# Kernel optimization log

Measured on AMD Instinct MI355X. Metric: run time of the kernel, lower is better.

## Reference

```python
import jax, jax.numpy as jnp
import numpy as np

WS = 7        # window_size
HEADS = 4     # dim_in // dim_head = 256 // 64
DH = 64       # dim_head (for q/k)
SCALE = DH ** -0.5


def setup_inputs() -> dict:
    key = jax.random.key(0)
    k1, k2, k3 = jax.random.split(key, 3)
    x = jax.random.normal(k1, (32, 256, 56, 56), dtype=jnp.float32)
    qk_w = jax.random.normal(k2, (512, 256), dtype=jnp.float32) * 0.02  # 1x1 conv: (out_c, in_c)
    v_w = jax.random.normal(k3, (256, 256), dtype=jnp.float32) * 0.02
    return {"x": x, "qk_w": qk_w, "v_w": v_w}


def _forward(x, qk_w, v_w):
    B, C, H, W = x.shape
    pad_b = (WS - H % WS) % WS
    pad_r = (WS - W % WS) % WS
    x = jnp.pad(x, ((0, 0), (0, 0), (0, pad_b), (0, pad_r)))
    Hp, Wp = H + pad_b, W + pad_r
    n1, n2 = Hp // WS, Wp // WS

    # 1x1 convs (no bias): qk -> 2*C channels, v -> dim_mid channels with ReLU
    qk = jnp.einsum('bchw,oc->bohw', x, qk_w)
    v = jax.nn.relu(jnp.einsum('bchw,oc->bohw', x, v_w))

    # remote (dilated grid) partition: 'b c (h1 n1) (w1 n2) -> (b n1 n2) c h1 w1'
    def part_r(t):
        b, c = t.shape[:2]
        return t.reshape(b, c, WS, n1, WS, n2).transpose(0, 3, 5, 1, 2, 4).reshape(b * n1 * n2, c, WS, WS)

    def merge_r(t, b):
        c = t.shape[1]
        return t.reshape(b, n1, n2, c, WS, WS).transpose(0, 3, 4, 1, 5, 2).reshape(b, c, Hp, Wp)

    # close (contiguous window) partition: 'b c (n1 h1) (n2 w1) -> (b n1 n2) c h1 w1'
    def part_c(t):
        b, c = t.shape[:2]
        return t.reshape(b, c, n1, WS, n2, WS).transpose(0, 2, 4, 1, 3, 5).reshape(b * n1 * n2, c, WS, WS)

    def merge_c(t, b):
        c = t.shape[1]
        return t.reshape(b, n1, n2, c, WS, WS).transpose(0, 3, 1, 4, 2, 5).reshape(b, c, Hp, Wp)

    def win_attn(qk_win, v_win):
        # qk_win: (bw, 2*HEADS*DH, WS, WS); channel order is (qk, heads, dim_head)
        bw = qk_win.shape[0]
        N = WS * WS
        qkr = qk_win.reshape(bw, 2, HEADS, DH, N)
        q = qkr[:, 0].transpose(0, 1, 3, 2)  # (bw, heads, N, DH)
        k = qkr[:, 1].transpose(0, 1, 3, 2)
        dhv = v_win.shape[1] // HEADS
        vv = v_win.reshape(bw, HEADS, dhv, N).transpose(0, 1, 3, 2)  # (bw, heads, N, dhv)
        attn = jax.nn.softmax(jnp.einsum('bhnd,bhmd->bhnm', q, k) * SCALE, axis=-1)
        o = jnp.einsum('bhnm,bhmd->bhnd', attn, vv)
        return o.transpose(0, 1, 3, 2).reshape(bw, HEADS * dhv, WS, WS)

    o_remote = merge_r(win_attn(part_r(qk), part_r(v)), B)
    o_close = merge_c(win_attn(part_c(qk), part_c(v)), B)
    out = o_remote + o_close
    return out[:, :, :H, :W]


def reference(x, qk_w, v_w):
    return _forward(x, qk_w, v_w)
```

## Files before the change

kernel.cpp:

```cpp
#include <hip/hip_runtime.h>
#include <stdint.h>


typedef float f32x4 __attribute__((ext_vector_type(4)));
typedef __attribute__((ext_vector_type(8))) short short8;

union V16 { uint4 u; short8 s; unsigned short h[8]; };

typedef const __attribute__((address_space(1))) uint32_t* gp_t;
typedef __attribute__((address_space(3))) uint32_t* lp_t;

__device__ __forceinline__ void async16(const void* g, void* l) {
  __builtin_amdgcn_global_load_lds((gp_t)g, (lp_t)l, 16, 0, 0);
}

__device__ __forceinline__ unsigned short f2bf(float f) {
  union { float f; uint32_t u; } a; a.f = f;
  uint32_t u = a.u;
  return (unsigned short)((u + 0x7FFFu + ((u >> 16) & 1u)) >> 16);
}

__device__ __forceinline__ unsigned short f2bf_rhu(float f) {
  union { float f; uint32_t u; } a; a.f = f;
  return (unsigned short)((a.u + 0x8000u) >> 16);
}

__device__ __forceinline__ float bf2f(uint32_t bits_hi16) {
  union { uint32_t u; float f; } a; a.u = bits_hi16; return a.f;
}

__global__ __launch_bounds__(256) void k_wconv(const float* __restrict__ qk_w,
                                               const float* __restrict__ v_w,
                                               unsigned short* __restrict__ Wb) {
  int i = blockIdx.x * 256 + threadIdx.x;
  int o = i >> 5, gidx = i & 31;
  int c0 = gidx * 8;
  const float* src = (o < 512) ? (qk_w + o * 256 + c0) : (v_w + (o - 512) * 256 + c0);
  unsigned short vv[8];
#pragma unroll
  for (int j = 0; j < 8; j++) vv[j] = f2bf(src[j]);
  uint4 u;
  u.x = (uint32_t)vv[0] | ((uint32_t)vv[1] << 16);
  u.y = (uint32_t)vv[2] | ((uint32_t)vv[3] << 16);
  u.z = (uint32_t)vv[4] | ((uint32_t)vv[5] << 16);
  u.w = (uint32_t)vv[6] | ((uint32_t)vv[7] << 16);
  int kb = gidx >> 3, gg = gidx & 7;
  char* dst = (char*)Wb + (size_t)o * 512 + kb * 128 + ((gg ^ (o & 7)) << 4);
  *(uint4*)dst = u;
}

__global__ __launch_bounds__(256) void k_xpose(const float* __restrict__ x,
                                               unsigned short* __restrict__ xT) {
  const int t = threadIdx.x;
  const int p = blockIdx.x * 64 + (t >> 2);
  const int sub = t & 3;
  const int c0 = blockIdx.y * 32 + sub * 8;
  const int b = blockIdx.z;
  const float* xp = x + ((size_t)(b * 256 + c0)) * 3136 + p;
  unsigned short vv[8];
#pragma unroll
  for (int j = 0; j < 8; j++) vv[j] = f2bf(xp[(size_t)j * 3136]);
  uint4 u;
  u.x = (uint32_t)vv[0] | ((uint32_t)vv[1] << 16);
  u.y = (uint32_t)vv[2] | ((uint32_t)vv[3] << 16);
  u.z = (uint32_t)vv[4] | ((uint32_t)vv[5] << 16);
  u.w = (uint32_t)vv[6] | ((uint32_t)vv[7] << 16);
  const int g = (c0 >> 3) & 7;
  const int kb = c0 >> 6;
  char* dst = (char*)xT + ((size_t)(b * 3136 + p)) * 512 + kb * 128 + ((g ^ (p & 7)) << 4);
  *(uint4*)dst = u;
}

__global__ __launch_bounds__(256) void k_conv(const unsigned short* __restrict__ Wb,
                                              const unsigned short* __restrict__ xT,
                                              unsigned short* __restrict__ qkv) {
  __shared__ uint4 lds4[2048];
  char* ldsA = (char*)lds4;
  char* ldsB = (char*)lds4 + 16384;
  const int bi = blockIdx.x;
  const int xcd = bi & 7, g = bi >> 3;
  const int bgrp = g / 150;
  const int rem = g - bgrp * 150;
  const int b = xcd + 8 * bgrp;
  const int ot = rem / 25;
  const int pt = rem - ot * 25;
  const int p0 = pt * 128, o0 = ot * 128;
  const bool isv = (ot >= 4);
  const float qs = (ot < 2) ? 0.18033688011112042f : 1.0f;

  const int tid = threadIdx.x;
  const int lane = tid & 63, wave = tid >> 6;
  const int lid = lane & 15, quad = lane >> 4;
  const int m_off = (wave & 1) * 64, n_off = (wave >> 1) * 64;
  const int psub = lane >> 3, chunk = lane & 7;
  const size_t rowb = (size_t)(b * 3136 + p0);
  const char* xTb = (const char*)xT;
  const char* Wbb = (const char*)Wb;

  f32x4 acc[4][4];
#pragma unroll
  for (int mi = 0; mi < 4; mi++)
#pragma unroll
    for (int ni = 0; ni < 4; ni++) { f32x4 z = {0.f, 0.f, 0.f, 0.f}; acc[mi][ni] = z; }

  for (int kk = 0; kk < 256; kk += 64) {
#pragma unroll
    for (int r = 0; r < 4; r++) {
      int i = wave * 4 + r;
      const char* ga = Wbb + (size_t)(o0 + i * 8 + psub) * 512 + kk * 2 + chunk * 16;
      async16(ga, ldsA + i * 1024);
      const char* gb = xTb + (rowb + i * 8 + psub) * 512 + kk * 2 + chunk * 16;
      async16(gb, ldsB + i * 1024);
    }
    __syncthreads();

    V16 a[4][2], bf[4][2];
#pragma unroll
    for (int mi = 0; mi < 4; mi++) {
      int ro = m_off + mi * 16 + lid;
#pragma unroll
      for (int ks = 0; ks < 2; ks++) {
        int gl = ks * 4 + quad;
        a[mi][ks].u = *(const uint4*)(ldsA + ro * 128 + ((gl ^ (ro & 7)) << 4));
      }
    }
#pragma unroll
    for (int ni = 0; ni < 4; ni++) {
      int px = n_off + ni * 16 + lid;
#pragma unroll
      for (int ks = 0; ks < 2; ks++) {
        int gl = ks * 4 + quad;
        bf[ni][ks].u = *(const uint4*)(ldsB + px * 128 + ((gl ^ (px & 7)) << 4));
      }
    }
#pragma unroll
    for (int mi = 0; mi < 4; mi++)
#pragma unroll
      for (int ni = 0; ni < 4; ni++) {
        acc[mi][ni] = __builtin_amdgcn_mfma_f32_16x16x32_bf16(a[mi][0].s, bf[ni][0].s, acc[mi][ni], 0, 0, 0);
        acc[mi][ni] = __builtin_amdgcn_mfma_f32_16x16x32_bf16(a[mi][1].s, bf[ni][1].s, acc[mi][ni], 0, 0, 0);
      }
    __syncthreads();
  }

#pragma unroll
  for (int mi = 0; mi < 4; mi++) {
    int o = o0 + m_off + mi * 16 + quad * 4;
#pragma unroll
    for (int ni = 0; ni < 4; ni++) {
      int px = p0 + n_off + ni * 16 + lid;
      if (px < 3136) {
        f32x4 v = acc[mi][ni];
        v.x *= qs; v.y *= qs; v.z *= qs; v.w *= qs;
        if (isv) {
          v.x = fmaxf(v.x, 0.f); v.y = fmaxf(v.y, 0.f);
          v.z = fmaxf(v.z, 0.f); v.w = fmaxf(v.w, 0.f);
        }
        ushort4 u;
        u.x = f2bf(v.x); u.y = f2bf(v.y); u.z = f2bf(v.z); u.w = f2bf(v.w);
        *(ushort4*)(qkv + ((size_t)(b * 3136 + px)) * 768 + o) = u;
      }
    }
  }
}

template <int PART, int FUSED>
__global__ __launch_bounds__(256) void k_attn_t(const unsigned short* __restrict__ qkv,
                                                const unsigned short* __restrict__ oPrev,
                                                unsigned short* __restrict__ oDst,
                                                float* __restrict__ out) {
  __shared__ uint4 smem4[2048];
  const int bi = blockIdx.x;
  const int xcd = bi & 7, g = bi >> 3;
  const int b = ((g >> 6) << 3) + xcd;
  const int w = g & 63;
  const int i1 = w >> 3, i2 = w & 7;
  const int off = PART ? (i1 * 392 + i2 * 7) : (i1 * 56 + i2);
  const int sh  = PART ? 56 : 448;
  const int sw  = PART ? 1 : 8;

  const int lane = threadIdx.x & 63;
  const int head = threadIdx.x >> 6;
  const int lid = lane & 15, quad = lane >> 4;
  char* Pb = (char*)smem4 + head * 8192;
  const unsigned short* __restrict__ qkvb = qkv + (size_t)b * 3136 * 768;

  auto pix = [&](int t) -> int {
    int h1 = (t * 37) >> 8;
    int w1 = t - h1 * 7;
    return off + h1 * sh + w1 * sw;
  };

  V16 va[4][2];
#pragma unroll
  for (int ks = 0; ks < 2; ks++)
#pragma unroll
    for (int j = 0; j < 8; j++) {
      int key = ks * 32 + quad * 8 + j;
      int p = pix(min(key, 48));
      const unsigned short* vp = qkvb + p * 768 + 512 + head * 64 + lid;
#pragma unroll
      for (int mi = 0; mi < 4; mi++) va[mi][ks].h[j] = vp[mi * 16];
    }

  V16 qf[4][2], kf[4][2];
#pragma unroll
  for (int mi = 0; mi < 4; mi++) {
    int p = pix(min(mi * 16 + lid, 48));
    const unsigned short* qp = qkvb + p * 768 + head * 64;
#pragma unroll
    for (int ks = 0; ks < 2; ks++) qf[mi][ks].u = *(const uint4*)(qp + ks * 32 + quad * 8);
  }
#pragma unroll
  for (int ni = 0; ni < 4; ni++) {
    int p = pix(min(ni * 16 + lid, 48));
    const unsigned short* kp = qkvb + p * 768 + 256 + head * 64;
#pragma unroll
    for (int ks = 0; ks < 2; ks++) kf[ni][ks].u = *(const uint4*)(kp + ks * 32 + quad * 8);
  }

  f32x4 s[4][4];
#pragma unroll
  for (int mi = 0; mi < 4; mi++)
#pragma unroll
    for (int ni = 0; ni < 4; ni++) {
      f32x4 z = {0.f, 0.f, 0.f, 0.f};
      z = __builtin_amdgcn_mfma_f32_16x16x32_bf16(kf[mi][0].s, qf[ni][0].s, z, 0, 0, 0);
      z = __builtin_amdgcn_mfma_f32_16x16x32_bf16(kf[mi][1].s, qf[ni][1].s, z, 0, 0, 0);
      s[mi][ni] = z;
    }

  {
    const int rx = lid & 7;
    char* wbase = Pb + lid * 128 + (quad & 1) * 8;
#pragma unroll
    for (int mi = 0; mi < 4; mi++) {
      const int swz = ((mi * 2 + (quad >> 1)) ^ rx) << 4;
#pragma unroll
      for (int ni = 0; ni < 4; ni++) {
        uint32_t d0, d1;
        if (mi < 3) {
          d0 = (uint32_t)f2bf_rhu(__builtin_amdgcn_exp2f(s[mi][ni][0]))
             | ((uint32_t)f2bf_rhu(__builtin_amdgcn_exp2f(s[mi][ni][1])) << 16);
          d1 = (uint32_t)f2bf_rhu(__builtin_amdgcn_exp2f(s[mi][ni][2]))
             | ((uint32_t)f2bf_rhu(__builtin_amdgcn_exp2f(s[mi][ni][3])) << 16);
        } else {
          d0 = quad ? 0u : (uint32_t)f2bf_rhu(__builtin_amdgcn_exp2f(s[3][ni][0]));
          d1 = 0u;
        }
        uint2 st; st.x = d0; st.y = d1;
        *(uint2*)(wbase + ni * 2048 + swz) = st;
      }
    }
  }
  __syncthreads();

  V16 pt[4][2];
#pragma unroll
  for (int ni = 0; ni < 4; ni++) {
    int row = ni * 16 + lid;
#pragma unroll
    for (int ks = 0; ks < 2; ks++) {
      int gl = ks * 4 + quad;
      pt[ni][ks].u = *(const uint4*)(Pb + row * 128 + ((gl ^ (row & 7)) << 4));
    }
  }

  V16 ones;
#pragma unroll
  for (int j = 0; j < 8; j++) ones.h[j] = 0x3F80;
  float inv[4];
  int pq[4]; bool qv[4];
#pragma unroll
  for (int ni = 0; ni < 4; ni++) {
    f32x4 z = {0.f, 0.f, 0.f, 0.f};
    z = __builtin_amdgcn_mfma_f32_16x16x32_bf16(ones.s, pt[ni][0].s, z, 0, 0, 0);
    z = __builtin_amdgcn_mfma_f32_16x16x32_bf16(ones.s, pt[ni][1].s, z, 0, 0, 0);
    inv[ni] = __builtin_amdgcn_rcpf(z[0]);
    int q = ni * 16 + lid;
    qv[ni] = q < 49;
    pq[ni] = pix(qv[ni] ? q : 48);
  }

#pragma unroll
  for (int mi = 0; mi < 4; mi++) {
    f32x4 om[4];
#pragma unroll
    for (int ni = 0; ni < 4; ni++) {
      f32x4 z = {0.f, 0.f, 0.f, 0.f};
      z = __builtin_amdgcn_mfma_f32_16x16x32_bf16(va[mi][0].s, pt[ni][0].s, z, 0, 0, 0);
      z = __builtin_amdgcn_mfma_f32_16x16x32_bf16(va[mi][1].s, pt[ni][1].s, z, 0, 0, 0);
      om[ni] = z;
    }
    if constexpr (!FUSED) {
      unsigned short* __restrict__ oSb = oDst + (size_t)b * 3136 * 256;
#pragma unroll
      for (int ni = 0; ni < 4; ni++) {
        if (qv[ni]) {
          float iv = inv[ni];
          uint32_t lo = ((uint32_t)f2bf_rhu(om[ni][0] * iv)) | ((uint32_t)f2bf_rhu(om[ni][1] * iv) << 16);
          uint32_t hi = ((uint32_t)f2bf_rhu(om[ni][2] * iv)) | ((uint32_t)f2bf_rhu(om[ni][3] * iv) << 16);
          uint2 st; st.x = lo; st.y = hi;
          *(uint2*)(oSb + pq[ni] * 256 + head * 64 + mi * 16 + quad * 4) = st;
        }
      }
    } else {
      const unsigned short* __restrict__ oPb = oPrev + (size_t)b * 3136 * 256;
      float* __restrict__ outb = out + (size_t)b * 256 * 3136;
      const int c0 = head * 64 + mi * 16 + quad * 4;
#pragma unroll
      for (int ni = 0; ni < 4; ni++) {
        if (qv[ni]) {
          float iv = inv[ni];
          uint2 r = *(const uint2*)(oPb + pq[ni] * 256 + c0);
          float o0 = om[ni][0] * iv + bf2f(r.x << 16);
          float o1 = om[ni][1] * iv + bf2f(r.x & 0xFFFF0000u);
          float o2 = om[ni][2] * iv + bf2f(r.y << 16);
          float o3 = om[ni][3] * iv + bf2f(r.y & 0xFFFF0000u);
          float* op = outb + (size_t)c0 * 3136 + pq[ni];
          op[0]        = o0;
          op[3136]     = o1;
          op[2 * 3136] = o2;
          op[3 * 3136] = o3;
        }
      }
    }
  }
}

extern "C" void kernel_launch(void* const* d_in, const int* in_sizes, int n_in,
                              void* d_out, int out_size, void* d_ws, size_t ws_size,
                              hipStream_t stream) {
  (void)in_sizes; (void)n_in; (void)out_size; (void)ws_size;
  const float* x    = (const float*)d_in[0];
  const float* qk_w = (const float*)d_in[1];
  const float* v_w  = (const float*)d_in[2];
  float* out = (float*)d_out;
  char* ws = (char*)d_ws;
  unsigned short* Wb  = (unsigned short*)ws;
  unsigned short* xT  = (unsigned short*)(ws + 393216);
  unsigned short* qkv = (unsigned short*)(ws + 51773440ull);
  unsigned short* oR  = xT;

  hipLaunchKernelGGL(k_wconv, dim3(96), dim3(256), 0, stream, qk_w, v_w, Wb);
  hipLaunchKernelGGL(k_xpose, dim3(49, 8, 32), dim3(256), 0, stream, x, xT);
  hipLaunchKernelGGL(k_conv, dim3(4800), dim3(256), 0, stream, Wb, xT, qkv);
  hipLaunchKernelGGL(HIP_KERNEL_NAME(k_attn_t<0, 0>), dim3(2048), dim3(256), 0, stream,
                     qkv, (const unsigned short*)nullptr, oR, (float*)nullptr);
  hipLaunchKernelGGL(HIP_KERNEL_NAME(k_attn_t<1, 1>), dim3(2048), dim3(256), 0, stream,
                     qkv, (const unsigned short*)oR, (unsigned short*)nullptr, out);
}
```

Measured before the change: 367.2 us.

## Double-buffer conv GEMM LDS loads and stage epilogue through LDS for coalesced stores

```diff
diff --git a/kernel.cpp b/kernel.cpp
--- a/kernel.cpp
+++ b/kernel.cpp
@@ -74,9 +74,8 @@
 __global__ __launch_bounds__(256) void k_conv(const unsigned short* __restrict__ Wb,
                                               const unsigned short* __restrict__ xT,
                                               unsigned short* __restrict__ qkv) {
-  __shared__ uint4 lds4[2048];
-  char* ldsA = (char*)lds4;
-  char* ldsB = (char*)lds4 + 16384;
+  __shared__ uint4 lds4[4096];
+  char* lds = (char*)lds4;
   const int bi = blockIdx.x;
   const int xcd = bi & 7, g = bi >> 3;
   const int bgrp = g / 150;
@@ -97,13 +96,9 @@
   const char* xTb = (const char*)xT;
   const char* Wbb = (const char*)Wb;
 
-  f32x4 acc[4][4];
-#pragma unroll
-  for (int mi = 0; mi < 4; mi++)
-#pragma unroll
-    for (int ni = 0; ni < 4; ni++) { f32x4 z = {0.f, 0.f, 0.f, 0.f}; acc[mi][ni] = z; }
-
-  for (int kk = 0; kk < 256; kk += 64) {
+  auto stage = [&](int kk, char* buf) {
+    char* ldsA = buf;
+    char* ldsB = buf + 16384;
 #pragma unroll
     for (int r = 0; r < 4; r++) {
       int i = wave * 4 + r;
@@ -112,7 +107,24 @@
       const char* gb = xTb + (rowb + i * 8 + psub) * 512 + kk * 2 + chunk * 16;
       async16(gb, ldsB + i * 1024);
     }
-    __syncthreads();
+  };
+
+  f32x4 acc[4][4];
+#pragma unroll
+  for (int mi = 0; mi < 4; mi++)
+#pragma unroll
+    for (int ni = 0; ni < 4; ni++) { f32x4 z = {0.f, 0.f, 0.f, 0.f}; acc[mi][ni] = z; }
+
+  stage(0, lds);
+  asm volatile("s_waitcnt vmcnt(0)" ::: "memory");
+  __builtin_amdgcn_s_barrier();
+
+#pragma unroll
+  for (int t = 0; t < 4; t++) {
+    char* cur = lds + (t & 1) * 32768;
+    if (t < 3) stage((t + 1) * 64, lds + ((t + 1) & 1) * 32768);
+    char* ldsA = cur;
+    char* ldsB = cur + 16384;
 
     V16 a[4][2], bf[4][2];
 #pragma unroll
@@ -140,27 +152,39 @@
         acc[mi][ni] = __builtin_amdgcn_mfma_f32_16x16x32_bf16(a[mi][0].s, bf[ni][0].s, acc[mi][ni], 0, 0, 0);
         acc[mi][ni] = __builtin_amdgcn_mfma_f32_16x16x32_bf16(a[mi][1].s, bf[ni][1].s, acc[mi][ni], 0, 0, 0);
       }
-    __syncthreads();
+
+    asm volatile("s_waitcnt vmcnt(0)" ::: "memory");
+    __builtin_amdgcn_s_barrier();
   }
 
 #pragma unroll
   for (int mi = 0; mi < 4; mi++) {
-    int o = o0 + m_off + mi * 16 + quad * 4;
+    const int chunkb = (m_off >> 3) + mi * 2 + (quad >> 1);
 #pragma unroll
     for (int ni = 0; ni < 4; ni++) {
-      int px = p0 + n_off + ni * 16 + lid;
-      if (px < 3136) {
-        f32x4 v = acc[mi][ni];
-        v.x *= qs; v.y *= qs; v.z *= qs; v.w *= qs;
-        if (isv) {
-          v.x = fmaxf(v.x, 0.f); v.y = fmaxf(v.y, 0.f);
-          v.z = fmaxf(v.z, 0.f); v.w = fmaxf(v.w, 0.f);
-        }
-        ushort4 u;
-        u.x = f2bf(v.x); u.y = f2bf(v.y); u.z = f2bf(v.z); u.w = f2bf(v.w);
-        *(ushort4*)(qkv + ((size_t)(b * 3136 + px)) * 768 + o) = u;
-      }
-    }
+      const int pxl = n_off + ni * 16 + lid;
+      f32x4 v = acc[mi][ni];
+      v.x *= qs; v.y *= qs; v.z *= qs; v.w *= qs;
+      if (isv) {
+        v.x = fmaxf(v.x, 0.f); v.y = fmaxf(v.y, 0.f);
+        v.z = fmaxf(v.z, 0.f); v.w = fmaxf(v.w, 0.f);
+      }
+      uint32_t lo = (uint32_t)f2bf(v.x) | ((uint32_t)f2bf(v.y) << 16);
+      uint32_t hi = (uint32_t)f2bf(v.z) | ((uint32_t)f2bf(v.w) << 16);
+      uint2 st; st.x = lo; st.y = hi;
+      *(uint2*)(lds + pxl * 256 + ((chunkb ^ (pxl & 7)) << 4) + (quad & 1) * 8) = st;
+    }
+  }
+  __syncthreads();
+
+#pragma unroll
+  for (int rep = 0; rep < 8; rep++) {
+    int idx = rep * 256 + tid;
+    int pxl = idx >> 4, seg = idx & 15;
+    uint4 vv = *(const uint4*)(lds + pxl * 256 + ((seg ^ (pxl & 7)) << 4));
+    int px = p0 + pxl;
+    if (px < 3136)
+      *(uint4*)((char*)qkv + ((size_t)(b * 3136 + px)) * 1536 + o0 * 2 + seg * 16) = vv;
   }
 }
 
```

Measured after the change: 361.2 us. No clear change (-1.6%).
